# Kernel tuning notes

Measured on AMD Instinct MI355X. Metric: run time of the kernel, lower is better.

## Reference

```python
import jax, jax.numpy as jnp
import numpy as np

EPS = 1e-7          # keras backend epsilon
BN_EPS = 1e-3       # keras BatchNormalization default epsilon
SCALES = (2, 4, 8, 16, 32)  # 2**i for i in 1..max_scale, max_scale=5


def _box_filter(x, k):
    # depthwise conv with all-ones k x k kernel, SAME padding (TF semantics)
    c = x.shape[-1]
    kern = jnp.ones((k, k, 1, c), x.dtype)
    return jax.lax.conv_general_dilated(
        x, kern, (1, 1), 'SAME',
        dimension_numbers=('NHWC', 'HWIO', 'NHWC'),
        feature_group_count=c)


def setup_inputs() -> dict:
    key = jax.random.key(0)
    ks = jax.random.split(key, 4)
    B, H, W, C, R = 16, 56, 56, 128, 8
    x = jax.random.normal(ks[0], (B, H, W, C), jnp.float32)
    kappa = jax.random.uniform(ks[1], (len(SCALES),), jnp.float32, -0.5, 0.5)
    W1 = jax.random.normal(ks[2], (C, C // R), jnp.float32) * (1.0 / np.sqrt(C))
    b1 = jnp.zeros((C // R,), jnp.float32)
    W2 = jax.random.normal(ks[3], (C // R, C), jnp.float32) * (1.0 / np.sqrt(C // R))
    b2 = jnp.zeros((C,), jnp.float32)
    gamma = jnp.ones((C,), jnp.float32)
    beta = jnp.zeros((C,), jnp.float32)
    bn_mean = jnp.zeros((C,), jnp.float32)
    bn_var = jnp.ones((C,), jnp.float32)
    return dict(x=x, kappa=kappa, W1=W1, b1=b1, W2=W2, b2=b2,
                gamma=gamma, beta=beta, bn_mean=bn_mean, bn_var=bn_var)


def reference(x, kappa, W1, b1, W2, b2, gamma, beta, bn_mean, bn_var):
    # per-sample min-max scaling over (H, W, C)
    xmin = jnp.min(x, axis=(1, 2, 3), keepdims=True)
    xmax = jnp.max(x, axis=(1, 2, 3), keepdims=True)
    xs = (x - xmin) / (xmax - xmin + EPS)

    # multi-scale box measures: [B,H,W,C,S]
    measures = jnp.stack([_box_filter(xs, k) for k in SCALES], axis=-1)
    log_m = jnp.log(measures + EPS)
    log_r = jnp.log(jnp.asarray(SCALES, jnp.float32))  # [S]

    # OLS slope of log_m vs log_r along scale axis -> alphas [B,H,W,C]
    xc = log_r - jnp.mean(log_r)
    alphas = jnp.sum(log_m * xc, axis=-1) / jnp.sum(xc * xc)

    # squeeze-and-excite on alphas
    squeeze = jnp.mean(alphas, axis=(1, 2))            # [B,C]
    hidden = jax.nn.relu(squeeze @ W1 + b1)            # [B,C//r]
    excite = jax.nn.sigmoid(hidden @ W2 + b2)          # [B,C]

    # weighted OLS estimate: alpha * (log_k + log_r) -> [B,H,W,C,S]
    k_ = jax.nn.sigmoid(kappa)
    log_k = jax.nn.sigmoid(jnp.log(k_ + EPS))          # [S]
    wols = alphas[..., None] * (log_k + log_r)

    # standardized (mean-centered) cosine similarity along scale axis, in [0,1]
    a = log_m - jnp.mean(log_m, axis=-1, keepdims=True)
    b = wols - jnp.mean(wols, axis=-1, keepdims=True)
    cos = jnp.sum(a * b, axis=-1) / (
        jnp.linalg.norm(a, axis=-1) * jnp.linalg.norm(b, axis=-1) + EPS)
    sim = 0.5 * (cos + 1.0)                            # [B,H,W,C]

    # inference-mode batchnorm on alphas
    alpha_norm = gamma * (alphas - bn_mean) * jax.lax.rsqrt(bn_var + BN_EPS) + beta

    x_exc = xs * excite[:, None, None, :]
    return sim * jax.nn.sigmoid(alpha_norm) + (1.0 - sim) * x_exc
```

## Files before the change

### kernel.cpp

```cpp
#include <hip/hip_runtime.h>
#include <hip/hip_fp16.h>

#define NTOT   6422528
#define NPERB  401408
#define NQ4    100352
#define SATR   228
#define LOG2E  1.4426950408889634f

__device__ __forceinline__ float sigmoidf_fast(float x) {
    return __builtin_amdgcn_rcpf(1.f + __expf(-x));
}

__device__ __forceinline__ unsigned encf(float f) {
    unsigned u = __float_as_uint(f);
    return (u & 0x80000000u) ? ~u : (u | 0x80000000u);
}
__device__ __forceinline__ float decf(unsigned u) {
    return __uint_as_float((u & 0x80000000u) ? (u ^ 0x80000000u) : ~u);
}

__device__ __forceinline__ void kappa_consts(const float* kap, float* dcs) {
    float v[5]; float mean = 0.f;
    for (int s = 0; s < 5; s++) {
        float lr = 0.6931471805599453f * (float)(s + 1);
        float k_ = 1.f / (1.f + expf(-kap[s]));
        float lk = 1.f / (1.f + expf(-logf(k_ + 1e-7f)));
        v[s] = lk + lr; mean += v[s];
    }
    mean *= 0.2f; float nd = 0.f;
    for (int s = 0; s < 5; s++) { float d = v[s] - mean; dcs[s] = d; nd += d * d; }
    dcs[5] = sqrtf(nd);
}

struct ScaleU { int rb1, rb0; float xmch; };

__global__ void k_minmax(const float4* __restrict__ x4,
                         unsigned* __restrict__ pmxu, unsigned* __restrict__ pmnn) {
    int p = blockIdx.x;
    int b = p & 15, chunk = p >> 4;
    const float4* base = x4 + b * NQ4 + chunk * 1568;
    float mx = -3.4e38f, mn = -3.4e38f;
    for (int q = threadIdx.x; q < 1568; q += 256) {
        float4 v = base[q];
        mx = fmaxf(mx, fmaxf(fmaxf(v.x, v.y), fmaxf(v.z, v.w)));
        mn = fmaxf(mn, fmaxf(fmaxf(-v.x, -v.y), fmaxf(-v.z, -v.w)));
    }
    __shared__ float rmx[4], rmn[4];
    int lane = threadIdx.x & 63, w = threadIdx.x >> 6;
#pragma unroll
    for (int off = 32; off; off >>= 1) {
        mx = fmaxf(mx, __shfl_down(mx, off));
        mn = fmaxf(mn, __shfl_down(mn, off));
    }
    if (lane == 0) { rmx[w] = mx; rmn[w] = mn; }
    __syncthreads();
    if (threadIdx.x == 0) {
        mx = fmaxf(fmaxf(rmx[0], rmx[1]), fmaxf(rmx[2], rmx[3]));
        mn = fmaxf(fmaxf(rmn[0], rmn[1]), fmaxf(rmn[2], rmn[3]));
        atomicMax(&pmxu[b], encf(mx));
        atomicMax(&pmnn[b], encf(mn));
    }
}

__launch_bounds__(896, 7)
__global__ void k_satg(const float* __restrict__ x,   const float* __restrict__ kap,
                       const float* __restrict__ gam, const float* __restrict__ bet,
                       const float* __restrict__ bnm, const float* __restrict__ bnv,
                       const unsigned* __restrict__ pmxu, const unsigned* __restrict__ pmnn,
                       float* __restrict__ sq, unsigned int* __restrict__ ABu) {
    __shared__ float SATl[57 * SATR];
    __shared__ float tot[896];
    __shared__ float wsum[56];
    __shared__ float cst[9];

    const int p = blockIdx.x;
    const int b = p & 15, cg = p >> 4;
    const int c0 = cg * 4;
    const int t = threadIdx.x;
    const int cc = t & 3;
    const int jrow = (t % 224) >> 2;
    const int seg = t / 224;

    if (t < 228) {
        SATl[t] = 0.f;
        SATl[(t >> 2) * SATR + (t & 3)] = 0.f;
    }
    if (t == 0) {
        float mxv = decf(pmxu[b]);
        float mnv = -decf(pmnn[b]);
        float xi = 1.f / (mxv - mnv + 1e-7f);
        cst[6] = mnv; cst[7] = xi; cst[8] = mnv * xi;
    } else if (t == 64) {
        float d[6]; kappa_consts(kap, d);
#pragma unroll
        for (int s2 = 0; s2 < 6; s2++) cst[s2] = d[s2];
    }

    float v[14];
    {
        const float* xp = x + b * NPERB + (seg * 14) * 7168 + jrow * 128 + c0 + cc;
        float acc = 0.f;
#pragma unroll
        for (int k = 0; k < 14; k++) { acc += xp[k * 7168]; v[k] = acc; }
        tot[t] = acc;
    }
    __syncthreads();
    {
        const int tj = jrow * 4 + cc;
        float base = 0.f;
        if (seg > 0) base += tot[tj];
        if (seg > 1) base += tot[224 + tj];
        if (seg > 2) base += tot[448 + tj];
#pragma unroll
        for (int k = 0; k < 14; k++)
            SATl[(seg * 14 + k + 1) * SATR + (jrow + 1) * 4 + cc] = base + v[k];
    }
    __syncthreads();

    {
        const int colbase = (jrow + 1) * SATR + cc;
#pragma unroll
        for (int k = 0; k < 14; k++) v[k] = SATl[colbase + (seg * 14 + 1 + k) * 4];
#pragma unroll
        for (int k = 1; k < 14; k++) v[k] += v[k - 1];
        tot[t] = v[13];
    }
    __syncthreads();
    {
        const int tj = jrow * 4 + cc;
        float base = 0.f;
        if (seg > 0) base += tot[tj];
        if (seg > 1) base += tot[224 + tj];
        if (seg > 2) base += tot[448 + tj];
        const int colbase = (jrow + 1) * SATR + cc;
#pragma unroll
        for (int k = 0; k < 14; k++)
            SATl[colbase + (seg * 14 + 1 + k) * 4] = base + v[k];
    }
    __syncthreads();

    float asum = 0.f;
    {
        const int i = jrow;
        const int j0 = seg * 14;
        const float xm = cst[6], xi = cst[7], xmxi = cst[8];
        const int ci = c0 + cc;
        const float g = gam[ci], be = bet[ci], bm = bnm[ci];
        const float rsv = rsqrtf(bnv[ci] + 1e-3f);
        const float A1c = g * rsv, A0c = be - g * bm * rsv;
        const float C1 = -A1c * (LOG2E * 0.1f);
        const float C0 = -A0c * LOG2E;
        const float d0 = cst[0], d1 = cst[1], d2 = cst[2], d3 = cst[3], d4 = cst[4], nd = cst[5];
        const float* sp = SATl + cc;

        auto mkU = [&](int hk) {
            ScaleU uu;
            int y1g = min(i + hk, 55) + 1;
            int y0g = max(i - hk + 1, 0);
            uu.rb1 = y1g * SATR; uu.rb0 = y0g * SATR;
            uu.xmch = xm * (float)(y1g - y0g);
            return uu;
        };
        const ScaleU u0 = mkU(1), u1 = mkU(2), u2 = mkU(4), u3 = mkU(8), u4 = mkU(16);

        auto meas = [&](int j, const ScaleU& uu, int hk) -> float {
            int x1g = min(j + hk, 55) + 1;
            int x0g = max(j - hk + 1, 0);
            float cw = (float)(x1g - x0g);
            int o1 = x1g << 2, o0 = x0g << 2;
            float s = sp[uu.rb1 + o1] - sp[uu.rb0 + o1] - sp[uu.rb1 + o0] + sp[uu.rb0 + o0];
            float t1 = fmaf(-uu.xmch, cw, s);
            return __log2f(fmaxf(fmaf(t1, xi, 1e-7f), 1e-7f));
        };

        const float* xrow = x + b * NPERB + i * 7168 + ci;
        unsigned int* abrow = ABu + b * NPERB + i * 7168 + ci;
        for (int jj = 0; jj < 14; jj++) {
            int j = j0 + jj;
            float l0 = meas(j, u0, 1);
            float l1 = meas(j, u1, 2);
            float l2 = meas(j, u2, 4);
            float l3 = meas(j, u3, 8);
            float l4 = meas(j, u4, 16);
            float w2 = -2.f * l0 - l1 + l3 + 2.f * l4;
            asum += w2;
            float alphas = w2 * 0.1f;
            float mean = 0.2f * (l0 + l1 + l2 + l3 + l4);
            float a0 = l0 - mean, a1 = l1 - mean, a2 = l2 - mean, a3 = l3 - mean, a4 = l4 - mean;
            float na2  = a0 * a0 + a1 * a1 + a2 * a2 + a3 * a3 + a4 * a4;
            float adot = a0 * d0 + a1 * d1 + a2 * d2 + a3 * d3 + a4 * d4;
            float na = __builtin_amdgcn_sqrtf(na2);
            float cosv = (alphas * adot) * __builtin_amdgcn_rcpf(na * fabsf(alphas) * nd + 1e-7f);
            float sim = 0.5f * (cosv + 1.f);
            float sbn = __builtin_amdgcn_rcpf(1.f + exp2f(C1 * w2 + C0));
            float xs = fmaf(xrow[j * 128], xi, -xmxi);
            float A = sim * sbn;
            float B = (1.f - sim) * xs;
            abrow[j * 128] = __builtin_bit_cast(unsigned int, __floats2half2_rn(A, B));
        }
    }
    asum += __shfl_down(asum, 32);
    asum += __shfl_down(asum, 16);
    asum += __shfl_down(asum, 8);
    asum += __shfl_down(asum, 4);
    if ((t & 63) < 4) wsum[(t >> 6) * 4 + (t & 3)] = asum;
    __syncthreads();
    if (t < 4) {
        float s = 0.f;
#pragma unroll
        for (int w = 0; w < 14; w++) s += wsum[w * 4 + t];
        atomicAdd(&sq[b * 128 + c0 + t], s * 0.1f);
    }
}

__launch_bounds__(256)
__global__ void k_mix(const unsigned int* __restrict__ ABu, const float* __restrict__ sq,
                      const float* __restrict__ W1, const float* __restrict__ b1,
                      const float* __restrict__ W2, const float* __restrict__ b2,
                      float* __restrict__ out) {
    __shared__ float sqz[128];
    __shared__ float hid[16];
    __shared__ float exc[128];
    int p = blockIdx.x;
    int b = p & 15, chunk = p >> 4;
    int tid = threadIdx.x;
    if (tid < 128) sqz[tid] = sq[b * 128 + tid] * (1.f / 3136.f);
    __syncthreads();
    if (tid < 16) {
        float acc = b1[tid];
        for (int c2 = 0; c2 < 128; c2++) acc += sqz[c2] * W1[c2 * 16 + tid];
        hid[tid] = fmaxf(acc, 0.f);
    }
    __syncthreads();
    if (tid < 128) {
        float acc = b2[tid];
#pragma unroll
        for (int h = 0; h < 16; h++) acc += hid[h] * W2[h * 128 + tid];
        exc[tid] = sigmoidf_fast(acc);
    }
    __syncthreads();
    const uint4* ab4 = (const uint4*)ABu + b * NQ4 + chunk * 784;
    float4* out4 = (float4*)out + b * NQ4 + chunk * 784;
    for (int q = tid; q < 784; q += 256) {
        int cb = ((chunk * 784 + q) & 31) << 2;
        uint4 u = ab4[q];
        float2 p0 = __half22float2(__builtin_bit_cast(__half2, u.x));
        float2 p1 = __half22float2(__builtin_bit_cast(__half2, u.y));
        float2 p2 = __half22float2(__builtin_bit_cast(__half2, u.z));
        float2 p3 = __half22float2(__builtin_bit_cast(__half2, u.w));
        out4[q] = make_float4(p0.x + p0.y * exc[cb],
                              p1.x + p1.y * exc[cb + 1],
                              p2.x + p2.y * exc[cb + 2],
                              p3.x + p3.y * exc[cb + 3]);
    }
}

extern "C" void kernel_launch(void* const* d_in, const int* in_sizes, int n_in,
                              void* d_out, int out_size, void* d_ws, size_t ws_size,
                              hipStream_t stream) {
    const float* x   = (const float*)d_in[0];
    const float* kap = (const float*)d_in[1];
    const float* W1  = (const float*)d_in[2];
    const float* b1  = (const float*)d_in[3];
    const float* W2  = (const float*)d_in[4];
    const float* b2  = (const float*)d_in[5];
    const float* gam = (const float*)d_in[6];
    const float* bet = (const float*)d_in[7];
    const float* bnm = (const float*)d_in[8];
    const float* bnv = (const float*)d_in[9];
    float* out = (float*)d_out;

    float*    sq   = (float*)d_ws;
    unsigned* pmxu = (unsigned*)(sq + 2048);
    unsigned* pmnn = pmxu + 16;
    unsigned* ABu  = (unsigned*)(sq + 2112);

    hipMemsetAsync(d_ws, 0, 8448, stream);
    k_minmax<<<1024, 256, 0, stream>>>((const float4*)x, pmxu, pmnn);
    k_satg<<<512, 896, 0, stream>>>(x, kap, gam, bet, bnm, bnv, pmxu, pmnn, sq, ABu);
    k_mix<<<2048, 256, 0, stream>>>(ABu, sq, W1, b1, W2, b2, out);
}
```

Before: 154.6 us.

## Restructure SAT kernel to two channels per block with float2 shared layout

```diff
diff --git a/kernel.cpp b/kernel.cpp
--- a/kernel.cpp
+++ b/kernel.cpp
@@ -4,7 +4,6 @@
 #define NTOT   6422528
 #define NPERB  401408
 #define NQ4    100352
-#define SATR   228
 #define LOG2E  1.4426950408889634f
 
 __device__ __forceinline__ float sigmoidf_fast(float x) {
@@ -62,153 +61,190 @@
     }
 }
 
-__launch_bounds__(896, 7)
+__launch_bounds__(448, 7)
 __global__ void k_satg(const float* __restrict__ x,   const float* __restrict__ kap,
                        const float* __restrict__ gam, const float* __restrict__ bet,
                        const float* __restrict__ bnm, const float* __restrict__ bnv,
                        const unsigned* __restrict__ pmxu, const unsigned* __restrict__ pmnn,
                        float* __restrict__ sq, unsigned int* __restrict__ ABu) {
-    __shared__ float SATl[57 * SATR];
-    __shared__ float tot[896];
-    __shared__ float wsum[56];
-    __shared__ float cst[9];
+    __shared__ float2 SAT2[57 * 57];
+    __shared__ float2 tot2[448];
+    __shared__ float  wsum[14];
+    __shared__ float  cst[9];
 
     const int p = blockIdx.x;
     const int b = p & 15, cg = p >> 4;
-    const int c0 = cg * 4;
+    const int c0 = cg * 2;
     const int t = threadIdx.x;
-    const int cc = t & 3;
-    const int jrow = (t % 224) >> 2;
-    const int seg = t / 224;
-
-    if (t < 228) {
-        SATl[t] = 0.f;
-        SATl[(t >> 2) * SATR + (t & 3)] = 0.f;
-    }
+    const int pos = t % 56;
+    const int seg = t / 56;
+
+    if (t < 57) SAT2[t] = make_float2(0.f, 0.f);
+    if (t >= 64 && t < 120) SAT2[(t - 63) * 57] = make_float2(0.f, 0.f);
     if (t == 0) {
         float mxv = decf(pmxu[b]);
         float mnv = -decf(pmnn[b]);
         float xi = 1.f / (mxv - mnv + 1e-7f);
         cst[6] = mnv; cst[7] = xi; cst[8] = mnv * xi;
-    } else if (t == 64) {
+    } else if (t == 128) {
         float d[6]; kappa_consts(kap, d);
 #pragma unroll
         for (int s2 = 0; s2 < 6; s2++) cst[s2] = d[s2];
     }
 
-    float v[14];
-    {
-        const float* xp = x + b * NPERB + (seg * 14) * 7168 + jrow * 128 + c0 + cc;
-        float acc = 0.f;
-#pragma unroll
-        for (int k = 0; k < 14; k++) { acc += xp[k * 7168]; v[k] = acc; }
-        tot[t] = acc;
-    }
-    __syncthreads();
-    {
-        const int tj = jrow * 4 + cc;
-        float base = 0.f;
-        if (seg > 0) base += tot[tj];
-        if (seg > 1) base += tot[224 + tj];
-        if (seg > 2) base += tot[448 + tj];
-#pragma unroll
-        for (int k = 0; k < 14; k++)
-            SATl[(seg * 14 + k + 1) * SATR + (jrow + 1) * 4 + cc] = base + v[k];
-    }
-    __syncthreads();
-
-    {
-        const int colbase = (jrow + 1) * SATR + cc;
-#pragma unroll
-        for (int k = 0; k < 14; k++) v[k] = SATl[colbase + (seg * 14 + 1 + k) * 4];
-#pragma unroll
-        for (int k = 1; k < 14; k++) v[k] += v[k - 1];
-        tot[t] = v[13];
-    }
-    __syncthreads();
-    {
-        const int tj = jrow * 4 + cc;
-        float base = 0.f;
-        if (seg > 0) base += tot[tj];
-        if (seg > 1) base += tot[224 + tj];
-        if (seg > 2) base += tot[448 + tj];
-        const int colbase = (jrow + 1) * SATR + cc;
-#pragma unroll
-        for (int k = 0; k < 14; k++)
-            SATl[colbase + (seg * 14 + 1 + k) * 4] = base + v[k];
-    }
-    __syncthreads();
-
-    float asum = 0.f;
-    {
-        const int i = jrow;
-        const int j0 = seg * 14;
+    float2 v[7];
+    {
+        const float2* xp = (const float2*)(x + b * NPERB + seg * 7 * 7168 + pos * 128 + c0);
+        float2 acc = make_float2(0.f, 0.f);
+#pragma unroll
+        for (int k = 0; k < 7; k++) {
+            float2 xv = xp[k * 3584];
+            acc.x += xv.x; acc.y += xv.y;
+            v[k] = acc;
+        }
+        tot2[t] = acc;
+    }
+    __syncthreads();
+    {
+        float2 base = make_float2(0.f, 0.f);
+        for (int s = 0; s < seg; s++) {
+            float2 tv = tot2[s * 56 + pos];
+            base.x += tv.x; base.y += tv.y;
+        }
+#pragma unroll
+        for (int k = 0; k < 7; k++)
+            SAT2[(seg * 7 + 1 + k) * 57 + (pos + 1)] =
+                make_float2(base.x + v[k].x, base.y + v[k].y);
+    }
+    __syncthreads();
+
+    {
+        const int rbase = (pos + 1) * 57 + seg * 7 + 1;
+#pragma unroll
+        for (int k = 0; k < 7; k++) v[k] = SAT2[rbase + k];
+#pragma unroll
+        for (int k = 1; k < 7; k++) { v[k].x += v[k - 1].x; v[k].y += v[k - 1].y; }
+        tot2[seg * 56 + pos] = v[6];
+    }
+    __syncthreads();
+    {
+        float2 base = make_float2(0.f, 0.f);
+        for (int s = 0; s < seg; s++) {
+            float2 tv = tot2[s * 56 + pos];
+            base.x += tv.x; base.y += tv.y;
+        }
+        const int rbase = (pos + 1) * 57 + seg * 7 + 1;
+#pragma unroll
+        for (int k = 0; k < 7; k++)
+            SAT2[rbase + k] = make_float2(base.x + v[k].x, base.y + v[k].y);
+    }
+    __syncthreads();
+
+    float asx = 0.f, asy = 0.f;
+    {
+        const int i = pos;
+        const int j0 = seg * 7;
         const float xm = cst[6], xi = cst[7], xmxi = cst[8];
-        const int ci = c0 + cc;
-        const float g = gam[ci], be = bet[ci], bm = bnm[ci];
-        const float rsv = rsqrtf(bnv[ci] + 1e-3f);
-        const float A1c = g * rsv, A0c = be - g * bm * rsv;
-        const float C1 = -A1c * (LOG2E * 0.1f);
-        const float C0 = -A0c * LOG2E;
         const float d0 = cst[0], d1 = cst[1], d2 = cst[2], d3 = cst[3], d4 = cst[4], nd = cst[5];
-        const float* sp = SATl + cc;
+        float C1x, C0x, C1y, C0y;
+        {
+            float g = gam[c0], be = bet[c0], bm = bnm[c0];
+            float rsv = rsqrtf(bnv[c0] + 1e-3f);
+            C1x = -(g * rsv) * (LOG2E * 0.1f);
+            C0x = -(be - g * bm * rsv) * LOG2E;
+            g = gam[c0 + 1]; be = bet[c0 + 1]; bm = bnm[c0 + 1];
+            rsv = rsqrtf(bnv[c0 + 1] + 1e-3f);
+            C1y = -(g * rsv) * (LOG2E * 0.1f);
+            C0y = -(be - g * bm * rsv) * LOG2E;
+        }
 
         auto mkU = [&](int hk) {
             ScaleU uu;
             int y1g = min(i + hk, 55) + 1;
             int y0g = max(i - hk + 1, 0);
-            uu.rb1 = y1g * SATR; uu.rb0 = y0g * SATR;
+            uu.rb1 = y1g * 57; uu.rb0 = y0g * 57;
             uu.xmch = xm * (float)(y1g - y0g);
             return uu;
         };
         const ScaleU u0 = mkU(1), u1 = mkU(2), u2 = mkU(4), u3 = mkU(8), u4 = mkU(16);
 
-        auto meas = [&](int j, const ScaleU& uu, int hk) -> float {
+        auto meas = [&](int j, const ScaleU& uu, int hk) -> float2 {
             int x1g = min(j + hk, 55) + 1;
             int x0g = max(j - hk + 1, 0);
             float cw = (float)(x1g - x0g);
-            int o1 = x1g << 2, o0 = x0g << 2;
-            float s = sp[uu.rb1 + o1] - sp[uu.rb0 + o1] - sp[uu.rb1 + o0] + sp[uu.rb0 + o0];
-            float t1 = fmaf(-uu.xmch, cw, s);
-            return __log2f(fmaxf(fmaf(t1, xi, 1e-7f), 1e-7f));
+            float2 a = SAT2[uu.rb1 + x1g], bq = SAT2[uu.rb0 + x1g];
+            float2 cq = SAT2[uu.rb1 + x0g], dq = SAT2[uu.rb0 + x0g];
+            float sx = a.x - bq.x - cq.x + dq.x;
+            float sy = a.y - bq.y - cq.y + dq.y;
+            float tx = fmaf(-uu.xmch, cw, sx);
+            float ty = fmaf(-uu.xmch, cw, sy);
+            float2 r;
+            r.x = __log2f(fmaxf(fmaf(tx, xi, 1e-7f), 1e-7f));
+            r.y = __log2f(fmaxf(fmaf(ty, xi, 1e-7f), 1e-7f));
+            return r;
         };
 
-        const float* xrow = x + b * NPERB + i * 7168 + ci;
-        unsigned int* abrow = ABu + b * NPERB + i * 7168 + ci;
-        for (int jj = 0; jj < 14; jj++) {
+        const float2* xrow = (const float2*)(x + b * NPERB + i * 7168 + c0);
+        uint2* abrow = (uint2*)(ABu + b * NPERB + i * 7168 + c0);
+        for (int jj = 0; jj < 7; jj++) {
             int j = j0 + jj;
-            float l0 = meas(j, u0, 1);
-            float l1 = meas(j, u1, 2);
-            float l2 = meas(j, u2, 4);
-            float l3 = meas(j, u3, 8);
-            float l4 = meas(j, u4, 16);
-            float w2 = -2.f * l0 - l1 + l3 + 2.f * l4;
-            asum += w2;
-            float alphas = w2 * 0.1f;
-            float mean = 0.2f * (l0 + l1 + l2 + l3 + l4);
-            float a0 = l0 - mean, a1 = l1 - mean, a2 = l2 - mean, a3 = l3 - mean, a4 = l4 - mean;
-            float na2  = a0 * a0 + a1 * a1 + a2 * a2 + a3 * a3 + a4 * a4;
-            float adot = a0 * d0 + a1 * d1 + a2 * d2 + a3 * d3 + a4 * d4;
-            float na = __builtin_amdgcn_sqrtf(na2);
-            float cosv = (alphas * adot) * __builtin_amdgcn_rcpf(na * fabsf(alphas) * nd + 1e-7f);
-            float sim = 0.5f * (cosv + 1.f);
-            float sbn = __builtin_amdgcn_rcpf(1.f + exp2f(C1 * w2 + C0));
-            float xs = fmaf(xrow[j * 128], xi, -xmxi);
-            float A = sim * sbn;
-            float B = (1.f - sim) * xs;
-            abrow[j * 128] = __builtin_bit_cast(unsigned int, __floats2half2_rn(A, B));
-        }
-    }
-    asum += __shfl_down(asum, 32);
-    asum += __shfl_down(asum, 16);
-    asum += __shfl_down(asum, 8);
-    asum += __shfl_down(asum, 4);
-    if ((t & 63) < 4) wsum[(t >> 6) * 4 + (t & 3)] = asum;
-    __syncthreads();
-    if (t < 4) {
+            float2 l0 = meas(j, u0, 1);
+            float2 l1 = meas(j, u1, 2);
+            float2 l2 = meas(j, u2, 4);
+            float2 l3 = meas(j, u3, 8);
+            float2 l4 = meas(j, u4, 16);
+            float2 xv = xrow[j * 64];
+            uint2 outw;
+            {
+                float w2 = -2.f * l0.x - l1.x + l3.x + 2.f * l4.x;
+                asx += w2;
+                float alphas = w2 * 0.1f;
+                float mean = 0.2f * (l0.x + l1.x + l2.x + l3.x + l4.x);
+                float a0 = l0.x - mean, a1 = l1.x - mean, a2 = l2.x - mean,
+                      a3 = l3.x - mean, a4 = l4.x - mean;
+                float na2  = a0 * a0 + a1 * a1 + a2 * a2 + a3 * a3 + a4 * a4;
+                float adot = a0 * d0 + a1 * d1 + a2 * d2 + a3 * d3 + a4 * d4;
+                float na = __builtin_amdgcn_sqrtf(na2);
+                float cosv = (alphas * adot) *
+                             __builtin_amdgcn_rcpf(na * fabsf(alphas) * nd + 1e-7f);
+                float sim = 0.5f * (cosv + 1.f);
+                float sbn = __builtin_amdgcn_rcpf(1.f + exp2f(C1x * w2 + C0x));
+                float xs = fmaf(xv.x, xi, -xmxi);
+                outw.x = __builtin_bit_cast(unsigned int,
+                          __floats2half2_rn(sim * sbn, (1.f - sim) * xs));
+            }
+            {
+                float w2 = -2.f * l0.y - l1.y + l3.y + 2.f * l4.y;
+                asy += w2;
+                float alphas = w2 * 0.1f;
+                float mean = 0.2f * (l0.y + l1.y + l2.y + l3.y + l4.y);
+                float a0 = l0.y - mean, a1 = l1.y - mean, a2 = l2.y - mean,
+                      a3 = l3.y - mean, a4 = l4.y - mean;
+                float na2  = a0 * a0 + a1 * a1 + a2 * a2 + a3 * a3 + a4 * a4;
+                float adot = a0 * d0 + a1 * d1 + a2 * d2 + a3 * d3 + a4 * d4;
+                float na = __builtin_amdgcn_sqrtf(na2);
+                float cosv = (alphas * adot) *
+                             __builtin_amdgcn_rcpf(na * fabsf(alphas) * nd + 1e-7f);
+                float sim = 0.5f * (cosv + 1.f);
+                float sbn = __builtin_amdgcn_rcpf(1.f + exp2f(C1y * w2 + C0y));
+                float xs = fmaf(xv.y, xi, -xmxi);
+                outw.y = __builtin_bit_cast(unsigned int,
+                          __floats2half2_rn(sim * sbn, (1.f - sim) * xs));
+            }
+            abrow[j * 64] = outw;
+        }
+    }
+#pragma unroll
+    for (int off = 32; off; off >>= 1) {
+        asx += __shfl_down(asx, off);
+        asy += __shfl_down(asy, off);
+    }
+    if ((t & 63) == 0) { wsum[(t >> 6) * 2] = asx; wsum[(t >> 6) * 2 + 1] = asy; }
+    __syncthreads();
+    if (t < 2) {
         float s = 0.f;
 #pragma unroll
-        for (int w = 0; w < 14; w++) s += wsum[w * 4 + t];
+        for (int w = 0; w < 7; w++) s += wsum[w * 2 + t];
         atomicAdd(&sq[b * 128 + c0 + t], s * 0.1f);
     }
 }
@@ -277,6 +313,6 @@
 
     hipMemsetAsync(d_ws, 0, 8448, stream);
     k_minmax<<<1024, 256, 0, stream>>>((const float4*)x, pmxu, pmnn);
-    k_satg<<<512, 896, 0, stream>>>(x, kap, gam, bet, bnm, bnv, pmxu, pmnn, sq, ABu);
+    k_satg<<<1024, 448, 0, stream>>>(x, kap, gam, bet, bnm, bnv, pmxu, pmnn, sq, ABu);
     k_mix<<<2048, 256, 0, stream>>>(ABu, sq, W1, b1, W2, b2, out);
 }
```

New measurement: 155.8 us. No clear change (+0.8%).
